# Optimization experiments

Hardware: AMD Instinct MI355X
Metric: run time of the kernel (lower is better)

The kernel has to match this reference:

```python
import jax, jax.numpy as jnp
import numpy as np

LAMBDA_MAX = 2.0  # standard re-scaled Laplacian assumption (DGL lambda_max=[2])
NUM_GRAPHS = 100


def _cheb(feat, src, dst, d_invsqrt, W, b):
    # DGL ChebConv: h = sum_i fc_i(X_i) + b, X_i = Chebyshev recursion on scaled Laplacian
    n = feat.shape[0]
    k = W.shape[0]
    re = 2.0 / LAMBDA_MAX

    def aggr(f):  # D^{-1/2} A D^{-1/2} f  via gather + segment_sum
        fh = f * d_invsqrt
        m = jax.ops.segment_sum(fh[src], dst, num_segments=n)
        return m * d_invsqrt

    X0 = feat
    h = X0 @ W[0]
    if k > 1:
        X1 = -re * aggr(X0) + X0 * (re - 1.0)
        h = h + X1 @ W[1]
        for i in range(2, k):
            Xi = -2.0 * re * aggr(X1) + X1 * (2.0 * (re - 1.0)) - X0
            h = h + Xi @ W[i]
            X0, X1 = X1, Xi
    return h + b


def _edgeconv(feat, src, dst, Wt, bt, Wp, bp):
    # DGL EdgeConv: out_i = max_{j->i} [theta(x_i - x_j) + phi(x_i)], 0 if no in-edges
    n = feat.shape[0]
    theta = (feat[dst] - feat[src]) @ Wt + bt           # [E, H]
    phi = feat @ Wp + bp                                # [N, H]
    msg = theta + phi[dst]                              # [E, H]
    agg = jax.ops.segment_max(msg, dst, num_segments=n)
    return jnp.where(jnp.isfinite(agg), agg, jnp.zeros((), feat.dtype))


def setup_inputs() -> dict:
    key = jax.random.key(0)
    ks = jax.random.split(key, 20)
    N, E, G = 100000, 1600000, NUM_GRAPHS
    IN, H, K = 16, 64, 3

    def lin(k, fan_in, shape):
        return jax.random.normal(k, shape, dtype=jnp.float32) * (1.0 / np.sqrt(fan_in))

    inp = {}
    inp["feat"] = jax.random.normal(ks[0], (N, IN), dtype=jnp.float32)
    inp["src"] = jax.random.randint(ks[1], (E,), 0, N)
    inp["dst"] = jax.random.randint(ks[2], (E,), 0, N)
    inp["graph_ids"] = jnp.sort(jax.random.randint(ks[3], (N,), 0, G))
    # ChebConv params: W [k, in, out], b [out]
    inp["W1"] = lin(ks[4], IN, (K, IN, H)); inp["b1"] = jnp.zeros((H,), jnp.float32)
    inp["W2"] = lin(ks[5], H, (K, H, H));   inp["b2"] = jnp.zeros((H,), jnp.float32)
    inp["W3"] = lin(ks[6], H, (K, H, H));   inp["b3"] = jnp.zeros((H,), jnp.float32)
    # EdgeConv params: theta + phi linears
    inp["Wt1"] = lin(ks[7], H, (H, H));  inp["bt1"] = jnp.zeros((H,), jnp.float32)
    inp["Wp1"] = lin(ks[8], H, (H, H));  inp["bp1"] = jnp.zeros((H,), jnp.float32)
    inp["Wt2"] = lin(ks[9], H, (H, H));  inp["bt2"] = jnp.zeros((H,), jnp.float32)
    inp["Wp2"] = lin(ks[10], H, (H, H)); inp["bp2"] = jnp.zeros((H,), jnp.float32)
    return inp


def reference(feat, src, dst, graph_ids, W1, b1, W2, b2, W3, b3,
              Wt1, bt1, Wp1, bp1, Wt2, bt2, Wp2, bp2):
    n = feat.shape[0]
    deg = jax.ops.segment_sum(jnp.ones((src.shape[0],), feat.dtype), dst, num_segments=n)
    d_invsqrt = (jnp.clip(deg, 1.0, None) ** -0.5)[:, None]  # [N, 1]

    h = jax.nn.relu(_cheb(feat, src, dst, d_invsqrt, W1, b1))
    h = jax.nn.relu(_edgeconv(h, src, dst, Wt1, bt1, Wp1, bp1))
    h = jax.nn.relu(_cheb(h, src, dst, d_invsqrt, W2, b2))
    h = jax.nn.relu(_edgeconv(h, src, dst, Wt2, bt2, Wp2, bp2))
    h = jax.nn.relu(_cheb(h, src, dst, d_invsqrt, W3, b3))

    # dgl.mean_nodes: per-graph mean pooling
    counts = jax.ops.segment_sum(jnp.ones((n,), h.dtype), graph_ids, num_segments=NUM_GRAPHS)
    hg = jax.ops.segment_sum(h, graph_ids, num_segments=NUM_GRAPHS)
    return hg / jnp.clip(counts, 1.0, None)[:, None]
```

## Files before the change

kernel.cpp:

```cpp
#include <hip/hip_runtime.h>
#include <hip/hip_bf16.h>
#include <math.h>

typedef __attribute__((ext_vector_type(8))) short short8;
typedef __attribute__((ext_vector_type(4))) float floatx4;

__device__ __forceinline__ unsigned short bfb(float x) {
    union { __hip_bfloat16 h; unsigned short u; } c;
    c.h = __float2bfloat16(x);
    return c.u;
}
__device__ __forceinline__ float bf2f(unsigned short u) {
    union { unsigned int i; float f; } c;
    c.i = ((unsigned int)u) << 16;
    return c.f;
}
__device__ __forceinline__ unsigned pkmaxu16(unsigned a, unsigned b) {
    unsigned d;
    asm("v_pk_max_u16 %0, %1, %2" : "=v"(d) : "v"(a), "v"(b));
    return d;
}


__global__ __launch_bounds__(256) void k_bhist(const int* __restrict__ dst, int* __restrict__ bcnt, int E) {
    __shared__ int h[512];
    int t = threadIdx.x;
    for (int i = t; i < 512; i += 256) h[i] = 0;
    __syncthreads();
    int step = gridDim.x * 256;
    for (int i = blockIdx.x * 256 + t; i < E; i += step) atomicAdd(&h[dst[i] >> 8], 1);
    __syncthreads();
    for (int i = t; i < 512; i += 256) if (h[i]) atomicAdd(&bcnt[i], h[i]);
}

__global__ __launch_bounds__(512) void k_scanBkt(const int* __restrict__ bcnt, int* __restrict__ boff,
                                                 int* __restrict__ bcur, int nb, int E) {
    __shared__ int s[512];
    int t = threadIdx.x;
    int v = (t < nb) ? bcnt[t] : 0;
    s[t] = v;
    __syncthreads();
    for (int off = 1; off < 512; off <<= 1) {
        int x = (t >= off) ? s[t - off] : 0;
        __syncthreads();
        s[t] += x;
        __syncthreads();
    }
    if (t < nb) { boff[t] = s[t] - v; bcur[t] = s[t] - v; }
    if (t == 0) boff[nb] = E;
}

#define PCHUNK 8192

__global__ __launch_bounds__(256) void k_partA(const int* __restrict__ src, const int* __restrict__ dst,
                                               int* __restrict__ bcur, unsigned* __restrict__ ebuf, int E) {
    __shared__ int h[512];
    __shared__ int base[512];
    int t = threadIdx.x;
    for (int i = t; i < 512; i += 256) h[i] = 0;
    __syncthreads();
    int start = blockIdx.x * PCHUNK;
    int end = start + PCHUNK < E ? start + PCHUNK : E;
    for (int i = start + t; i < end; i += 256) atomicAdd(&h[dst[i] >> 8], 1);
    __syncthreads();
    for (int i = t; i < 512; i += 256) {
        int c = h[i];
        base[i] = c ? atomicAdd(&bcur[i], c) : 0;
        h[i] = 0;
    }
    __syncthreads();
    for (int i = start + t; i < end; i += 256) {
        int d = dst[i];
        int b = d >> 8;
        int r = atomicAdd(&h[b], 1);
        ebuf[base[b] + r] = ((unsigned)src[i] << 8) | (unsigned)(d & 255);
    }
}

__global__ __launch_bounds__(256) void k_finish(const unsigned* __restrict__ ebuf, const int* __restrict__ boff,
                                                int* __restrict__ row_off, float* __restrict__ dinv,
                                                int* __restrict__ csr, int N, int E) {
    __shared__ int h[256];
    __shared__ int sc[256];
    __shared__ int cur[256];
    int b = blockIdx.x, t = threadIdx.x;
    h[t] = 0;
    __syncthreads();
    int beg = boff[b], end = boff[b + 1];
    for (int e = beg + t; e < end; e += 256) atomicAdd(&h[ebuf[e] & 255], 1);
    __syncthreads();
    int v = h[t];
    sc[t] = v;
    __syncthreads();
    for (int off = 1; off < 256; off <<= 1) {
        int x = (t >= off) ? sc[t - off] : 0;
        __syncthreads();
        sc[t] += x;
        __syncthreads();
    }
    int node = (b << 8) + t;
    int excl = beg + sc[t] - v;
    if (node < N) {
        row_off[node] = excl;
        dinv[node] = rsqrtf((float)(v > 1 ? v : 1));
    }
    cur[t] = excl;
    if (b == 0 && t == 0) row_off[N] = E;
    __syncthreads();
    for (int e = beg + t; e < end; e += 256) {
        unsigned ed = ebuf[e];
        int pos = atomicAdd(&cur[ed & 255], 1);
        csr[pos] = (int)(ed >> 8);
    }
}


__global__ __launch_bounds__(256) void k_feat16(const float* __restrict__ feat, const float* __restrict__ dinv,
                                                unsigned short* __restrict__ featd, int total) {
    int i = blockIdx.x * 256 + threadIdx.x;
    if (i < total) featd[i] = bfb(feat[i] * dinv[i >> 4]);
}


__global__ __launch_bounds__(256) void k_aggr16(const unsigned short* __restrict__ Xd, const float* __restrict__ Z,
                                                const float* __restrict__ dinv,
                                                const int* __restrict__ row_off, const int* __restrict__ csr,
                                                float* __restrict__ out, unsigned short* __restrict__ outd,
                                                float alpha, float beta, int N) {
    int node = blockIdx.x * 4 + (threadIdx.x >> 6);
    if (node >= N) return;
    int lane = threadIdx.x & 63;
    int g = lane >> 2;
    int co = (lane & 3) * 8;
    int beg = row_off[node], end = row_off[node + 1];
    int deg = end - beg;
    int myOff = ((lane < deg) ? csr[beg + lane] : 0) << 5;
    int dmain = deg < 64 ? deg : 64;
    float a0 = 0.f, a1 = 0.f, a2 = 0.f, a3 = 0.f;
    int j = 0;
    for (; j + 15 < dmain; j += 16) {
        int off = __shfl(myOff, j + g);
        ushort4 x = *(const ushort4*)((const char*)Xd + off + co);
        a0 += bf2f(x.x); a1 += bf2f(x.y); a2 += bf2f(x.z); a3 += bf2f(x.w);
    }
    if (j < dmain) {
        int idx = j + g;
        int off = __shfl(myOff, idx < dmain ? idx : dmain - 1);
        ushort4 x = *(const ushort4*)((const char*)Xd + off + co);
        if (idx < dmain) {
            a0 += bf2f(x.x); a1 += bf2f(x.y); a2 += bf2f(x.z); a3 += bf2f(x.w);
        }
    }
    for (int e = beg + 64; e < end; e += 16) {
        int idx = e + g;
        int s = csr[idx < end ? idx : end - 1];
        ushort4 x = *(const ushort4*)((const char*)Xd + (s << 5) + co);
        if (idx < end) {
            a0 += bf2f(x.x); a1 += bf2f(x.y); a2 += bf2f(x.z); a3 += bf2f(x.w);
        }
    }
    a0 += __shfl_xor(a0, 4); a0 += __shfl_xor(a0, 8); a0 += __shfl_xor(a0, 16); a0 += __shfl_xor(a0, 32);
    a1 += __shfl_xor(a1, 4); a1 += __shfl_xor(a1, 8); a1 += __shfl_xor(a1, 16); a1 += __shfl_xor(a1, 32);
    a2 += __shfl_xor(a2, 4); a2 += __shfl_xor(a2, 8); a2 += __shfl_xor(a2, 16); a2 += __shfl_xor(a2, 32);
    a3 += __shfl_xor(a3, 4); a3 += __shfl_xor(a3, 8); a3 += __shfl_xor(a3, 16); a3 += __shfl_xor(a3, 32);
    if (g == 0) {
        int c4 = (lane & 3) * 4;
        float dn = dinv[node];
        float v0 = alpha * dn * a0;
        float v1 = alpha * dn * a1;
        float v2 = alpha * dn * a2;
        float v3 = alpha * dn * a3;
        if (Z) {
            float4 zv = *(const float4*)&Z[(size_t)node * 16 + c4];
            v0 += beta * zv.x; v1 += beta * zv.y; v2 += beta * zv.z; v3 += beta * zv.w;
        }
        float4 r = { v0, v1, v2, v3 };
        *(float4*)&out[(size_t)node * 16 + c4] = r;
        if (outd) {
            ushort4 u = { bfb(v0 * dn), bfb(v1 * dn), bfb(v2 * dn), bfb(v3 * dn) };
            *(ushort4*)&outd[(size_t)node * 16 + c4] = u;
        }
    }
}


__global__ __launch_bounds__(256) void k_aggr64(const unsigned short* __restrict__ Xd, const float* __restrict__ Z,
                                                const float* __restrict__ dinv,
                                                const int* __restrict__ row_off, const int* __restrict__ csr,
                                                unsigned short* __restrict__ outb, unsigned short* __restrict__ outd,
                                                float alpha, float beta, int N) {
    int node = blockIdx.x * 4 + (threadIdx.x >> 6);
    if (node >= N) return;
    int lane = threadIdx.x & 63;
    int g = lane >> 4;
    int co = (lane & 15) * 8;
    int beg = row_off[node], end = row_off[node + 1];
    int deg = end - beg;
    int myOff = ((lane < deg) ? csr[beg + lane] : 0) << 7;
    int dmain = deg < 64 ? deg : 64;
    float a0 = 0.f, a1 = 0.f, a2 = 0.f, a3 = 0.f;
    float b0 = 0.f, b1 = 0.f, b2 = 0.f, b3 = 0.f;
    int j = 0;
    for (; j + 15 < dmain; j += 16) {
        int oA = __shfl(myOff, j + g);
        int oB = __shfl(myOff, j + 4 + g);
        int oC = __shfl(myOff, j + 8 + g);
        int oD = __shfl(myOff, j + 12 + g);
        ushort4 xA = *(const ushort4*)((const char*)Xd + oA + co);
        ushort4 xB = *(const ushort4*)((const char*)Xd + oB + co);
        ushort4 xC = *(const ushort4*)((const char*)Xd + oC + co);
        ushort4 xD = *(const ushort4*)((const char*)Xd + oD + co);
        a0 += bf2f(xA.x); a1 += bf2f(xA.y); a2 += bf2f(xA.z); a3 += bf2f(xA.w);
        b0 += bf2f(xB.x); b1 += bf2f(xB.y); b2 += bf2f(xB.z); b3 += bf2f(xB.w);
        a0 += bf2f(xC.x); a1 += bf2f(xC.y); a2 += bf2f(xC.z); a3 += bf2f(xC.w);
        b0 += bf2f(xD.x); b1 += bf2f(xD.y); b2 += bf2f(xD.z); b3 += bf2f(xD.w);
    }
    for (; j + 7 < dmain; j += 8) {
        int oA = __shfl(myOff, j + g);
        int oB = __shfl(myOff, j + 4 + g);
        ushort4 xA = *(const ushort4*)((const char*)Xd + oA + co);
        ushort4 xB = *(const ushort4*)((const char*)Xd + oB + co);
        a0 += bf2f(xA.x); a1 += bf2f(xA.y); a2 += bf2f(xA.z); a3 += bf2f(xA.w);
        b0 += bf2f(xB.x); b1 += bf2f(xB.y); b2 += bf2f(xB.z); b3 += bf2f(xB.w);
    }
    for (; j < dmain; j += 4) {
        int idx = j + g;
        int off = __shfl(myOff, idx < dmain ? idx : dmain - 1);
        ushort4 x = *(const ushort4*)((const char*)Xd + off + co);
        if (idx < dmain) {
            a0 += bf2f(x.x); a1 += bf2f(x.y); a2 += bf2f(x.z); a3 += bf2f(x.w);
        }
    }
    for (int e = beg + 64; e < end; e += 4) {
        int idx = e + g;
        int s = csr[idx < end ? idx : end - 1];
        ushort4 x = *(const ushort4*)((const char*)Xd + (s << 7) + co);
        if (idx < end) {
            a0 += bf2f(x.x); a1 += bf2f(x.y); a2 += bf2f(x.z); a3 += bf2f(x.w);
        }
    }
    a0 += b0; a1 += b1; a2 += b2; a3 += b3;
    a0 += __shfl_xor(a0, 16); a0 += __shfl_xor(a0, 32);
    a1 += __shfl_xor(a1, 16); a1 += __shfl_xor(a1, 32);
    a2 += __shfl_xor(a2, 16); a2 += __shfl_xor(a2, 32);
    a3 += __shfl_xor(a3, 16); a3 += __shfl_xor(a3, 32);
    if (g == 0) {
        int c4 = (lane & 15) * 4;
        float dn = dinv[node];
        float v0 = alpha * dn * a0;
        float v1 = alpha * dn * a1;
        float v2 = alpha * dn * a2;
        float v3 = alpha * dn * a3;
        if (Z) {
            float4 zv = *(const float4*)&Z[(size_t)node * 64 + c4];
            v0 += beta * zv.x; v1 += beta * zv.y; v2 += beta * zv.z; v3 += beta * zv.w;
        }
        ushort4 ub = { bfb(v0), bfb(v1), bfb(v2), bfb(v3) };
        *(ushort4*)&outb[(size_t)node * 64 + c4] = ub;
        if (outd) {
            ushort4 u = { bfb(v0 * dn), bfb(v1 * dn), bfb(v2 * dn), bfb(v3 * dn) };
            *(ushort4*)&outd[(size_t)node * 64 + c4] = u;
        }
    }
}


template <int KDIM, bool BIN16, bool BOUT16>
__global__ __launch_bounds__(256) void k_cheb_m(const float* __restrict__ X0, const void* __restrict__ X1v,
                                                const void* __restrict__ X2v, const float* __restrict__ W,
                                                const float* __restrict__ b, void* __restrict__ outv, int N) {
    constexpr int KT = (KDIM == 16) ? 64 : 3 * KDIM;
    constexpr int SX = KT + 8;
    __shared__ unsigned short Xs[64 * SX];
    __shared__ unsigned short Ws[64 * SX];
    int t = threadIdx.x;

    {
        int sn = t & 63;
        int gn = blockIdx.x * 64 + sn; if (gn >= N) gn = N - 1;
        int k0 = (t >> 6) * (KDIM / 4);
#pragma unroll
        for (int i = 0; i < KDIM / 16; ++i) {
            float4 v = *(const float4*)&X0[(size_t)gn * KDIM + k0 + 4 * i];
            ushort4 u = { bfb(v.x), bfb(v.y), bfb(v.z), bfb(v.w) };
            *(ushort4*)&Xs[sn * SX + k0 + 4 * i] = u;
        }
        if constexpr (BIN16) {
            const unsigned short* X1 = (const unsigned short*)X1v;
            const unsigned short* X2 = (const unsigned short*)X2v;
#pragma unroll
            for (int i = 0; i < KDIM / 16; ++i) {
                *(ushort4*)&Xs[sn * SX + KDIM + k0 + 4 * i] =
                    *(const ushort4*)&X1[(size_t)gn * KDIM + k0 + 4 * i];
                *(ushort4*)&Xs[sn * SX + 2 * KDIM + k0 + 4 * i] =
                    *(const ushort4*)&X2[(size_t)gn * KDIM + k0 + 4 * i];
            }
        } else {
            const float* Xp[2] = { (const float*)X1v, (const float*)X2v };
#pragma unroll
            for (int a = 0; a < 2; ++a) {
#pragma unroll
                for (int i = 0; i < KDIM / 16; ++i) {
                    float4 v = *(const float4*)&Xp[a][(size_t)gn * KDIM + k0 + 4 * i];
                    ushort4 u = { bfb(v.x), bfb(v.y), bfb(v.z), bfb(v.w) };
                    *(ushort4*)&Xs[sn * SX + (a + 1) * KDIM + k0 + 4 * i] = u;
                }
            }
        }
        if (KDIM == 16) {
            int kp = 48 + (t >> 6) * 4;
            ushort4 z = { 0, 0, 0, 0 };
            *(ushort4*)&Xs[sn * SX + kp] = z;
        }
    }
    for (int idx = t; idx < 3 * KDIM * 64; idx += 256) {
        int a = idx / (KDIM * 64);
        int r = idx % (KDIM * 64);
        int k = r >> 6, n = r & 63;
        Ws[n * SX + a * KDIM + k] = bfb(W[idx]);
    }
    if (KDIM == 16) {
        for (int idx = t; idx < 1024; idx += 256) {
            int n = idx & 63, k = 48 + (idx >> 6);
            Ws[n * SX + k] = 0;
        }
    }
    __syncthreads();

    int wave = t >> 6, lane = t & 63;
    int fi = lane & 15, quad = lane >> 4;
    int arow = wave * 16 + fi;

    floatx4 acc0 = {0.f,0.f,0.f,0.f}, acc1 = {0.f,0.f,0.f,0.f}, acc2 = {0.f,0.f,0.f,0.f}, acc3 = {0.f,0.f,0.f,0.f};
#pragma unroll
    for (int ks = 0; ks < KT / 32; ++ks) {
        short8 af = *(const short8*)&Xs[arow * SX + ks * 32 + quad * 8];
        short8 b0 = *(const short8*)&Ws[(0 * 16 + fi) * SX + ks * 32 + quad * 8];
        short8 b1 = *(const short8*)&Ws[(1 * 16 + fi) * SX + ks * 32 + quad * 8];
        short8 b2 = *(const short8*)&Ws[(2 * 16 + fi) * SX + ks * 32 + quad * 8];
        short8 b3 = *(const short8*)&Ws[(3 * 16 + fi) * SX + ks * 32 + quad * 8];
        acc0 = __builtin_amdgcn_mfma_f32_16x16x32_bf16(af, b0, acc0, 0, 0, 0);
        acc1 = __builtin_amdgcn_mfma_f32_16x16x32_bf16(af, b1, acc1, 0, 0, 0);
        acc2 = __builtin_amdgcn_mfma_f32_16x16x32_bf16(af, b2, acc2, 0, 0, 0);
        acc3 = __builtin_amdgcn_mfma_f32_16x16x32_bf16(af, b3, acc3, 0, 0, 0);
    }

    int nbase = blockIdx.x * 64 + wave * 16 + quad * 4;
    floatx4 accs[4] = { acc0, acc1, acc2, acc3 };
#pragma unroll
    for (int nt = 0; nt < 4; ++nt) {
        int col = nt * 16 + fi;
        float bias = b[col];
#pragma unroll
        for (int reg = 0; reg < 4; ++reg) {
            int node = nbase + reg;
            if (node < N) {
                float r = fmaxf(accs[nt][reg] + bias, 0.f);
                if constexpr (BOUT16) {
                    ((unsigned short*)outv)[(size_t)node * 64 + col] = bfb(r);
                } else {
                    ((float*)outv)[(size_t)node * 64 + col] = r;
                }
            }
        }
    }
}


__global__ __launch_bounds__(256) void k_e1_m(const unsigned short* X, const float* __restrict__ Wt,
                                              const float* __restrict__ Wp, const float* __restrict__ bt,
                                              const float* __restrict__ bp,
                                              unsigned short* md, float* __restrict__ pbuf, int N) {
    constexpr int SX = 72;
    __shared__ unsigned short Xs[64 * SX];
    __shared__ unsigned short Ws[128 * SX];
    int t = threadIdx.x;

    {
        int sn = t & 63;
        int gn = blockIdx.x * 64 + sn; if (gn >= N) gn = N - 1;
        int k0 = (t >> 6) * 16;
#pragma unroll
        for (int i = 0; i < 2; ++i) {
            *(short8*)&Xs[sn * SX + k0 + 8 * i] = *(const short8*)&X[(size_t)gn * 64 + k0 + 8 * i];
        }
    }
    for (int idx = t; idx < 4096; idx += 256) {
        int k = idx >> 6, n = idx & 63;
        float wt = Wt[idx];
        Ws[n * SX + k] = bfb(wt);
        Ws[(64 + n) * SX + k] = bfb(wt + Wp[idx]);
    }
    __syncthreads();

    int wave = t >> 6, lane = t & 63;
    int fi = lane & 15, quad = lane >> 4;
    int arow = wave * 16 + fi;

    floatx4 acc[8];
#pragma unroll
    for (int i = 0; i < 8; ++i) acc[i] = (floatx4){0.f,0.f,0.f,0.f};
#pragma unroll
    for (int ks = 0; ks < 2; ++ks) {
        short8 af = *(const short8*)&Xs[arow * SX + ks * 32 + quad * 8];
#pragma unroll
        for (int nt = 0; nt < 8; ++nt) {
            short8 bf = *(const short8*)&Ws[(nt * 16 + fi) * SX + ks * 32 + quad * 8];
            acc[nt] = __builtin_amdgcn_mfma_f32_16x16x32_bf16(af, bf, acc[nt], 0, 0, 0);
        }
    }

    int nbase = blockIdx.x * 64 + wave * 16 + quad * 4;
#pragma unroll
    for (int nt = 0; nt < 8; ++nt) {
        int col = nt * 16 + fi;
        if (col < 64) {
#pragma unroll
            for (int reg = 0; reg < 4; ++reg) {
                int node = nbase + reg;
                if (node < N) {
                    unsigned u = (unsigned)bfb(acc[nt][reg]) ^ 0x8000u;
                    unsigned key = (u & 0x8000u) ? (~u & 0xffffu) : (u | 0x8000u);
                    md[(size_t)node * 64 + col] = (unsigned short)key;
                }
            }
        } else {
            int cc = col - 64;
            float bias = bt[cc] + bp[cc];
#pragma unroll
            for (int reg = 0; reg < 4; ++reg) {
                int node = nbase + reg;
                if (node < N) pbuf[(size_t)node * 64 + cc] = acc[nt][reg] + bias;
            }
        }
    }
}


__global__ __launch_bounds__(256) void k_e2_b(const unsigned short* __restrict__ md, const float* __restrict__ pbuf,
                                              const int* __restrict__ row_off, const int* __restrict__ csr,
                                              const float* __restrict__ dinv, float* __restrict__ out,
                                              unsigned short* __restrict__ outd, int N) {
    int node = blockIdx.x * 4 + (threadIdx.x >> 6);
    if (node >= N) return;
    int lane = threadIdx.x & 63;
    int g = lane >> 4;
    int co = (lane & 15) * 8;
    int beg = row_off[node], end = row_off[node + 1];
    int deg = end - beg;
    int myOff = ((lane < deg) ? csr[beg + lane] : 0) << 7;
    int dmain = deg < 64 ? deg : 64;
    unsigned kA0 = 0, kA1 = 0, kB0 = 0, kB1 = 0;
    int j = 0;
    for (; j + 15 < dmain; j += 16) {
        int oA = __shfl(myOff, j + g);
        int oB = __shfl(myOff, j + 4 + g);
        int oC = __shfl(myOff, j + 8 + g);
        int oD = __shfl(myOff, j + 12 + g);
        uint2 xA = *(const uint2*)((const char*)md + oA + co);
        uint2 xB = *(const uint2*)((const char*)md + oB + co);
        uint2 xC = *(const uint2*)((const char*)md + oC + co);
        uint2 xD = *(const uint2*)((const char*)md + oD + co);
        kA0 = pkmaxu16(kA0, xA.x); kA1 = pkmaxu16(kA1, xA.y);
        kB0 = pkmaxu16(kB0, xB.x); kB1 = pkmaxu16(kB1, xB.y);
        kA0 = pkmaxu16(kA0, xC.x); kA1 = pkmaxu16(kA1, xC.y);
        kB0 = pkmaxu16(kB0, xD.x); kB1 = pkmaxu16(kB1, xD.y);
    }
    for (; j + 7 < dmain; j += 8) {
        int oA = __shfl(myOff, j + g);
        int oB = __shfl(myOff, j + 4 + g);
        uint2 xA = *(const uint2*)((const char*)md + oA + co);
        uint2 xB = *(const uint2*)((const char*)md + oB + co);
        kA0 = pkmaxu16(kA0, xA.x); kA1 = pkmaxu16(kA1, xA.y);
        kB0 = pkmaxu16(kB0, xB.x); kB1 = pkmaxu16(kB1, xB.y);
    }
    for (; j < dmain; j += 4) {
        int idx = j + g;
        int off = __shfl(myOff, idx < dmain ? idx : dmain - 1);
        uint2 x = *(const uint2*)((const char*)md + off + co);
        kA0 = pkmaxu16(kA0, idx < dmain ? x.x : 0u);
        kA1 = pkmaxu16(kA1, idx < dmain ? x.y : 0u);
    }
    for (int e = beg + 64; e < end; e += 4) {
        int idx = e + g;
        int s = csr[idx < end ? idx : end - 1];
        uint2 x = *(const uint2*)((const char*)md + (s << 7) + co);
        kA0 = pkmaxu16(kA0, idx < end ? x.x : 0u);
        kA1 = pkmaxu16(kA1, idx < end ? x.y : 0u);
    }
    kA0 = pkmaxu16(kA0, kB0); kA1 = pkmaxu16(kA1, kB1);
    kA0 = pkmaxu16(kA0, __shfl_xor((int)kA0, 16)); kA0 = pkmaxu16(kA0, __shfl_xor((int)kA0, 32));
    kA1 = pkmaxu16(kA1, __shfl_xor((int)kA1, 16)); kA1 = pkmaxu16(kA1, __shfl_xor((int)kA1, 32));
    if (g == 0) {
        int c4 = (lane & 15) * 4;
        unsigned short ks[4] = { (unsigned short)(kA0 & 0xffff), (unsigned short)(kA0 >> 16),
                                 (unsigned short)(kA1 & 0xffff), (unsigned short)(kA1 >> 16) };
        float a[4];
#pragma unroll
        for (int i = 0; i < 4; ++i) {
            unsigned k = ks[i];
            unsigned short tt = (k & 0x8000u) ? (unsigned short)(k & 0x7fffu) : (unsigned short)(~k & 0xffffu);
            a[i] = bf2f(tt);
        }
        float r0 = 0.f, r1 = 0.f, r2 = 0.f, r3 = 0.f;
        if (end > beg) {
            float4 pv = *(const float4*)&pbuf[(size_t)node * 64 + c4];
            r0 = fmaxf(pv.x + a[0], 0.f);
            r1 = fmaxf(pv.y + a[1], 0.f);
            r2 = fmaxf(pv.z + a[2], 0.f);
            r3 = fmaxf(pv.w + a[3], 0.f);
        }
        float4 r = { r0, r1, r2, r3 };
        *(float4*)&out[(size_t)node * 64 + c4] = r;
        float dn = dinv[node];
        ushort4 u = { bfb(r0 * dn), bfb(r1 * dn), bfb(r2 * dn), bfb(r3 * dn) };
        *(ushort4*)&outd[(size_t)node * 64 + c4] = u;
    }
}


__global__ __launch_bounds__(256) void k_pool(const float* __restrict__ h, const int* __restrict__ gid,
                                              float* __restrict__ out, float* __restrict__ gcnt, int N) {
    const int CHUNK = 128;
    int wave = blockIdx.x * 4 + (threadIdx.x >> 6);
    int lane = threadIdx.x & 63;
    int beg = wave * CHUNK;
    if (beg >= N) return;
    int end = beg + CHUNK < N ? beg + CHUNK : N;
    int gcur = gid[beg];
    float acc = 0.f;
    int cnt = 0;
    for (int n = beg; n < end; ++n) {
        int g = gid[n];
        float v = h[n * 64 + lane];
        if (g != gcur) {
            atomicAdd(&out[gcur * 64 + lane], acc);
            if (lane == 0) atomicAdd(&gcnt[gcur], (float)cnt);
            gcur = g; acc = 0.f; cnt = 0;
        }
        acc += v;
        ++cnt;
    }
    atomicAdd(&out[gcur * 64 + lane], acc);
    if (lane == 0) atomicAdd(&gcnt[gcur], (float)cnt);
}

__global__ __launch_bounds__(256) void k_div(float* __restrict__ out, const float* __restrict__ gcnt, int total) {
    int i = blockIdx.x * blockDim.x + threadIdx.x;
    if (i < total) out[i] /= fmaxf(gcnt[i >> 6], 1.f);
}


extern "C" void kernel_launch(void* const* d_in, const int* in_sizes, int n_in,
                              void* d_out, int out_size, void* d_ws, size_t ws_size,
                              hipStream_t stream) {
    const float* feat = (const float*)d_in[0];
    const int* src = (const int*)d_in[1];
    const int* dst = (const int*)d_in[2];
    const int* gid = (const int*)d_in[3];
    const float* W1 = (const float*)d_in[4];  const float* b1 = (const float*)d_in[5];
    const float* W2 = (const float*)d_in[6];  const float* b2 = (const float*)d_in[7];
    const float* W3 = (const float*)d_in[8];  const float* b3 = (const float*)d_in[9];
    const float* Wt1 = (const float*)d_in[10]; const float* bt1 = (const float*)d_in[11];
    const float* Wp1 = (const float*)d_in[12]; const float* bp1 = (const float*)d_in[13];
    const float* Wt2 = (const float*)d_in[14]; const float* bt2 = (const float*)d_in[15];
    const float* Wp2 = (const float*)d_in[16]; const float* bp2 = (const float*)d_in[17];
    float* out = (float*)d_out;

    const int N = in_sizes[0] / 16;
    const int E = in_sizes[1];
    const int G = out_size / 64;
    const int nb = (N + 255) >> 8;

    char* p = (char*)d_ws;
    auto alloc = [&](size_t nbytes) {
        void* r = (void*)p;
        p += (nbytes + 255) & ~(size_t)255;
        return r;
    };
    int* row_off  = (int*)alloc((size_t)(N + 1) * 4);
    int* csr      = (int*)alloc((size_t)E * 4);
    int* bcnt     = (int*)alloc(512 * 4);
    int* boff     = (int*)alloc(513 * 4);
    int* bcur     = (int*)alloc(512 * 4);
    float* dinv   = (float*)alloc((size_t)N * 4);
    float* bufA   = (float*)alloc((size_t)N * 64 * 4);
    float* bufB   = (float*)alloc((size_t)N * 64 * 4);
    float* bufC   = (float*)alloc((size_t)N * 64 * 4);
    float* bufD   = (float*)alloc((size_t)N * 64 * 4);
    unsigned short* md = (unsigned short*)alloc((size_t)N * 64 * 2);
    float* gcnt   = (float*)alloc((size_t)G * 4);

    unsigned* ebuf = (unsigned*)bufA;
    unsigned short* hd = (unsigned short*)bufC;
    unsigned short* xd = (unsigned short*)bufC + (size_t)N * 64;
    unsigned short* hb = md;

    hipMemsetAsync(bcnt, 0, 512 * 4, stream);
    hipMemsetAsync(gcnt, 0, (size_t)G * 4, stream);
    hipMemsetAsync(d_out, 0, (size_t)out_size * 4, stream);

    const int nb16 = (N * 16 + 255) / 256;
    const int nbw = (N + 3) / 4;
    const int npool = ((N + 127) / 128 + 3) / 4;
    const int nbt = (N + 63) / 64;
    const int npart = (E + PCHUNK - 1) / PCHUNK;

    k_bhist<<<256, 256, 0, stream>>>(dst, bcnt, E);
    k_scanBkt<<<1, 512, 0, stream>>>(bcnt, boff, bcur, nb, E);
    k_partA<<<npart, 256, 0, stream>>>(src, dst, bcur, ebuf, E);
    k_finish<<<nb, 256, 0, stream>>>(ebuf, boff, row_off, dinv, csr, N, E);

    k_feat16<<<nb16, 256, 0, stream>>>(feat, dinv, hd, N * 16);
    k_aggr16<<<nbw, 256, 0, stream>>>(hd, nullptr, dinv, row_off, csr, bufA, xd, -1.f, 0.f, N);
    k_aggr16<<<nbw, 256, 0, stream>>>(xd, feat, dinv, row_off, csr, bufB, nullptr, -2.f, -1.f, N);
    k_cheb_m<16, false, true><<<nbt, 256, 0, stream>>>(feat, bufA, bufB, W1, b1, hb, N);

    k_e1_m<<<nbt, 256, 0, stream>>>(hb, Wt1, Wp1, bt1, bp1, md, bufB, N);
    k_e2_b<<<nbw, 256, 0, stream>>>(md, bufB, row_off, csr, dinv, bufD, hd, N);

    k_aggr64<<<nbw, 256, 0, stream>>>(hd, nullptr, dinv, row_off, csr, (unsigned short*)bufA, xd, -1.f, 0.f, N);
    k_aggr64<<<nbw, 256, 0, stream>>>(xd, bufD, dinv, row_off, csr, (unsigned short*)bufB, nullptr, -2.f, -1.f, N);
    k_cheb_m<64, true, true><<<nbt, 256, 0, stream>>>(bufD, bufA, bufB, W2, b2, hb, N);

    k_e1_m<<<nbt, 256, 0, stream>>>(hb, Wt2, Wp2, bt2, bp2, md, bufB, N);
    k_e2_b<<<nbw, 256, 0, stream>>>(md, bufB, row_off, csr, dinv, bufD, hd, N);

    k_aggr64<<<nbw, 256, 0, stream>>>(hd, nullptr, dinv, row_off, csr, (unsigned short*)bufA, xd, -1.f, 0.f, N);
    k_aggr64<<<nbw, 256, 0, stream>>>(xd, bufD, dinv, row_off, csr, (unsigned short*)bufB, nullptr, -2.f, -1.f, N);
    k_cheb_m<64, true, false><<<nbt, 256, 0, stream>>>(bufD, bufA, bufB, W3, b3, bufC, N);

    k_pool<<<npool, 256, 0, stream>>>(bufC, gid, out, gcnt, N);
    k_div<<<(out_size + 255) / 256, 256, 0, stream>>>(out, gcnt, out_size);
}
```

Measured before the change: 621.3 us.

## Widen gather loads to 16 bytes, use zero-page padding, store edge output as bf16

The 64-wide aggregation and edge-max kernels now let each lane load 16 bytes per neighbor (8 lanes per row) instead of 8 bytes. Lanes past the degree point at a zeroed scratch page, so the first 32 neighbors are gathered unconditionally without masking. The edge-conv output and the Chebyshev X0 input are now stored in bf16 rather than fp32, which halves that traffic. The aim is fewer, wider memory transactions and less branching, at the cost of wasted loads for nodes with few neighbors and some extra bf16 rounding.

```diff
diff --git a/kernel.cpp b/kernel.cpp
--- a/kernel.cpp
+++ b/kernel.cpp
@@ -14,6 +14,12 @@
     union { unsigned int i; float f; } c;
     c.i = ((unsigned int)u) << 16;
     return c.f;
+}
+__device__ __forceinline__ void acc2(float& lo, float& hi, unsigned d) {
+    union { unsigned u; float f; } a, b;
+    a.u = d << 16;
+    b.u = d & 0xffff0000u;
+    lo += a.f; hi += b.f;
 }
 __device__ __forceinline__ unsigned pkmaxu16(unsigned a, unsigned b) {
     unsigned d;
@@ -126,7 +132,7 @@
                                                 const float* __restrict__ dinv,
                                                 const int* __restrict__ row_off, const int* __restrict__ csr,
                                                 float* __restrict__ out, unsigned short* __restrict__ outd,
-                                                float alpha, float beta, int N) {
+                                                float alpha, float beta, int zoff, int N) {
     int node = blockIdx.x * 4 + (threadIdx.x >> 6);
     if (node >= N) return;
     int lane = threadIdx.x & 63;
@@ -134,29 +140,31 @@
     int co = (lane & 3) * 8;
     int beg = row_off[node], end = row_off[node + 1];
     int deg = end - beg;
-    int myOff = ((lane < deg) ? csr[beg + lane] : 0) << 5;
-    int dmain = deg < 64 ? deg : 64;
+    int myOff = (lane < deg) ? (csr[beg + lane] << 5) : zoff;
+    const char* base = (const char*)Xd + co;
     float a0 = 0.f, a1 = 0.f, a2 = 0.f, a3 = 0.f;
-    int j = 0;
-    for (; j + 15 < dmain; j += 16) {
-        int off = __shfl(myOff, j + g);
-        ushort4 x = *(const ushort4*)((const char*)Xd + off + co);
-        a0 += bf2f(x.x); a1 += bf2f(x.y); a2 += bf2f(x.z); a3 += bf2f(x.w);
-    }
-    if (j < dmain) {
-        int idx = j + g;
-        int off = __shfl(myOff, idx < dmain ? idx : dmain - 1);
-        ushort4 x = *(const ushort4*)((const char*)Xd + off + co);
-        if (idx < dmain) {
+    {
+        int o0 = __shfl(myOff, g);
+        int o1 = __shfl(myOff, 16 + g);
+        ushort4 x0 = *(const ushort4*)(base + o0);
+        ushort4 x1 = *(const ushort4*)(base + o1);
+        a0 += bf2f(x0.x); a1 += bf2f(x0.y); a2 += bf2f(x0.z); a3 += bf2f(x0.w);
+        a0 += bf2f(x1.x); a1 += bf2f(x1.y); a2 += bf2f(x1.z); a3 += bf2f(x1.w);
+    }
+    if (deg > 32) {
+        int dmain = deg < 64 ? deg : 64;
+        for (int j = 32; j < dmain; j += 16) {
+            int o = __shfl(myOff, j + g);
+            ushort4 x = *(const ushort4*)(base + o);
             a0 += bf2f(x.x); a1 += bf2f(x.y); a2 += bf2f(x.z); a3 += bf2f(x.w);
         }
-    }
-    for (int e = beg + 64; e < end; e += 16) {
-        int idx = e + g;
-        int s = csr[idx < end ? idx : end - 1];
-        ushort4 x = *(const ushort4*)((const char*)Xd + (s << 5) + co);
-        if (idx < end) {
-            a0 += bf2f(x.x); a1 += bf2f(x.y); a2 += bf2f(x.z); a3 += bf2f(x.w);
+        for (int e = beg + 64; e < end; e += 16) {
+            int idx = e + g;
+            int s = csr[idx < end ? idx : end - 1];
+            ushort4 x = *(const ushort4*)(base + (s << 5));
+            if (idx < end) {
+                a0 += bf2f(x.x); a1 += bf2f(x.y); a2 += bf2f(x.z); a3 += bf2f(x.w);
+            }
         }
     }
     a0 += __shfl_xor(a0, 4); a0 += __shfl_xor(a0, 8); a0 += __shfl_xor(a0, 16); a0 += __shfl_xor(a0, 32);
@@ -184,89 +192,93 @@
 }
 
 
-__global__ __launch_bounds__(256) void k_aggr64(const unsigned short* __restrict__ Xd, const float* __restrict__ Z,
+__global__ __launch_bounds__(256) void k_aggr64(const unsigned short* __restrict__ Xd,
+                                                const unsigned short* __restrict__ Z,
                                                 const float* __restrict__ dinv,
                                                 const int* __restrict__ row_off, const int* __restrict__ csr,
                                                 unsigned short* __restrict__ outb, unsigned short* __restrict__ outd,
-                                                float alpha, float beta, int N) {
+                                                float alpha, float beta, int zoff, int N) {
     int node = blockIdx.x * 4 + (threadIdx.x >> 6);
     if (node >= N) return;
     int lane = threadIdx.x & 63;
-    int g = lane >> 4;
-    int co = (lane & 15) * 8;
+    int g = lane >> 3;
+    int co = (lane & 7) * 16;
     int beg = row_off[node], end = row_off[node + 1];
     int deg = end - beg;
-    int myOff = ((lane < deg) ? csr[beg + lane] : 0) << 7;
-    int dmain = deg < 64 ? deg : 64;
-    float a0 = 0.f, a1 = 0.f, a2 = 0.f, a3 = 0.f;
-    float b0 = 0.f, b1 = 0.f, b2 = 0.f, b3 = 0.f;
-    int j = 0;
-    for (; j + 15 < dmain; j += 16) {
-        int oA = __shfl(myOff, j + g);
-        int oB = __shfl(myOff, j + 4 + g);
-        int oC = __shfl(myOff, j + 8 + g);
-        int oD = __shfl(myOff, j + 12 + g);
-        ushort4 xA = *(const ushort4*)((const char*)Xd + oA + co);
-        ushort4 xB = *(const ushort4*)((const char*)Xd + oB + co);
-        ushort4 xC = *(const ushort4*)((const char*)Xd + oC + co);
-        ushort4 xD = *(const ushort4*)((const char*)Xd + oD + co);
-        a0 += bf2f(xA.x); a1 += bf2f(xA.y); a2 += bf2f(xA.z); a3 += bf2f(xA.w);
-        b0 += bf2f(xB.x); b1 += bf2f(xB.y); b2 += bf2f(xB.z); b3 += bf2f(xB.w);
-        a0 += bf2f(xC.x); a1 += bf2f(xC.y); a2 += bf2f(xC.z); a3 += bf2f(xC.w);
-        b0 += bf2f(xD.x); b1 += bf2f(xD.y); b2 += bf2f(xD.z); b3 += bf2f(xD.w);
-    }
-    for (; j + 7 < dmain; j += 8) {
-        int oA = __shfl(myOff, j + g);
-        int oB = __shfl(myOff, j + 4 + g);
-        ushort4 xA = *(const ushort4*)((const char*)Xd + oA + co);
-        ushort4 xB = *(const ushort4*)((const char*)Xd + oB + co);
-        a0 += bf2f(xA.x); a1 += bf2f(xA.y); a2 += bf2f(xA.z); a3 += bf2f(xA.w);
-        b0 += bf2f(xB.x); b1 += bf2f(xB.y); b2 += bf2f(xB.z); b3 += bf2f(xB.w);
-    }
-    for (; j < dmain; j += 4) {
-        int idx = j + g;
-        int off = __shfl(myOff, idx < dmain ? idx : dmain - 1);
-        ushort4 x = *(const ushort4*)((const char*)Xd + off + co);
-        if (idx < dmain) {
-            a0 += bf2f(x.x); a1 += bf2f(x.y); a2 += bf2f(x.z); a3 += bf2f(x.w);
-        }
-    }
-    for (int e = beg + 64; e < end; e += 4) {
-        int idx = e + g;
-        int s = csr[idx < end ? idx : end - 1];
-        ushort4 x = *(const ushort4*)((const char*)Xd + (s << 7) + co);
-        if (idx < end) {
-            a0 += bf2f(x.x); a1 += bf2f(x.y); a2 += bf2f(x.z); a3 += bf2f(x.w);
-        }
-    }
-    a0 += b0; a1 += b1; a2 += b2; a3 += b3;
-    a0 += __shfl_xor(a0, 16); a0 += __shfl_xor(a0, 32);
-    a1 += __shfl_xor(a1, 16); a1 += __shfl_xor(a1, 32);
-    a2 += __shfl_xor(a2, 16); a2 += __shfl_xor(a2, 32);
-    a3 += __shfl_xor(a3, 16); a3 += __shfl_xor(a3, 32);
+    int myOff = (lane < deg) ? (csr[beg + lane] << 7) : zoff;
+    const char* base = (const char*)Xd + co;
+    float a0 = 0.f, a1 = 0.f, a2 = 0.f, a3 = 0.f, a4 = 0.f, a5 = 0.f, a6 = 0.f, a7 = 0.f;
+    {
+        int o0 = __shfl(myOff, g);
+        int o1 = __shfl(myOff, 8 + g);
+        int o2 = __shfl(myOff, 16 + g);
+        int o3 = __shfl(myOff, 24 + g);
+        uint4 x0 = *(const uint4*)(base + o0);
+        uint4 x1 = *(const uint4*)(base + o1);
+        uint4 x2 = *(const uint4*)(base + o2);
+        uint4 x3 = *(const uint4*)(base + o3);
+        acc2(a0, a1, x0.x); acc2(a2, a3, x0.y); acc2(a4, a5, x0.z); acc2(a6, a7, x0.w);
+        acc2(a0, a1, x1.x); acc2(a2, a3, x1.y); acc2(a4, a5, x1.z); acc2(a6, a7, x1.w);
+        acc2(a0, a1, x2.x); acc2(a2, a3, x2.y); acc2(a4, a5, x2.z); acc2(a6, a7, x2.w);
+        acc2(a0, a1, x3.x); acc2(a2, a3, x3.y); acc2(a4, a5, x3.z); acc2(a6, a7, x3.w);
+    }
+    if (deg > 32) {
+        int dmain = deg < 64 ? deg : 64;
+        for (int j = 32; j < dmain; j += 8) {
+            int o = __shfl(myOff, j + g);
+            uint4 x = *(const uint4*)(base + o);
+            acc2(a0, a1, x.x); acc2(a2, a3, x.y); acc2(a4, a5, x.z); acc2(a6, a7, x.w);
+        }
+        for (int e = beg + 64; e < end; e += 8) {
+            int idx = e + g;
+            int s = csr[idx < end ? idx : end - 1];
+            uint4 x = *(const uint4*)(base + (s << 7));
+            if (idx < end) {
+                acc2(a0, a1, x.x); acc2(a2, a3, x.y); acc2(a4, a5, x.z); acc2(a6, a7, x.w);
+            }
+        }
+    }
+    a0 += __shfl_xor(a0, 8); a0 += __shfl_xor(a0, 16); a0 += __shfl_xor(a0, 32);
+    a1 += __shfl_xor(a1, 8); a1 += __shfl_xor(a1, 16); a1 += __shfl_xor(a1, 32);
+    a2 += __shfl_xor(a2, 8); a2 += __shfl_xor(a2, 16); a2 += __shfl_xor(a2, 32);
+    a3 += __shfl_xor(a3, 8); a3 += __shfl_xor(a3, 16); a3 += __shfl_xor(a3, 32);
+    a4 += __shfl_xor(a4, 8); a4 += __shfl_xor(a4, 16); a4 += __shfl_xor(a4, 32);
+    a5 += __shfl_xor(a5, 8); a5 += __shfl_xor(a5, 16); a5 += __shfl_xor(a5, 32);
+    a6 += __shfl_xor(a6, 8); a6 += __shfl_xor(a6, 16); a6 += __shfl_xor(a6, 32);
+    a7 += __shfl_xor(a7, 8); a7 += __shfl_xor(a7, 16); a7 += __shfl_xor(a7, 32);
     if (g == 0) {
-        int c4 = (lane & 15) * 4;
         float dn = dinv[node];
-        float v0 = alpha * dn * a0;
-        float v1 = alpha * dn * a1;
-        float v2 = alpha * dn * a2;
-        float v3 = alpha * dn * a3;
+        float v[8] = { a0, a1, a2, a3, a4, a5, a6, a7 };
+#pragma unroll
+        for (int i = 0; i < 8; ++i) v[i] *= alpha * dn;
+        size_t rb = (size_t)node * 128 + co;
         if (Z) {
-            float4 zv = *(const float4*)&Z[(size_t)node * 64 + c4];
-            v0 += beta * zv.x; v1 += beta * zv.y; v2 += beta * zv.z; v3 += beta * zv.w;
-        }
-        ushort4 ub = { bfb(v0), bfb(v1), bfb(v2), bfb(v3) };
-        *(ushort4*)&outb[(size_t)node * 64 + c4] = ub;
-        if (outd) {
-            ushort4 u = { bfb(v0 * dn), bfb(v1 * dn), bfb(v2 * dn), bfb(v3 * dn) };
-            *(ushort4*)&outd[(size_t)node * 64 + c4] = u;
-        }
+            uint4 zv = *(const uint4*)((const char*)Z + rb);
+            unsigned zd[4] = { zv.x, zv.y, zv.z, zv.w };
+#pragma unroll
+            for (int i = 0; i < 4; ++i) {
+                union { unsigned u; float f; } lo, hi;
+                lo.u = zd[i] << 16; hi.u = zd[i] & 0xffff0000u;
+                v[2 * i] += beta * lo.f;
+                v[2 * i + 1] += beta * hi.f;
+            }
+        }
+        uint4 ub, ud;
+        unsigned* pb = (unsigned*)&ub;
+        unsigned* pd = (unsigned*)&ud;
+#pragma unroll
+        for (int i = 0; i < 4; ++i) {
+            pb[i] = (unsigned)bfb(v[2 * i]) | ((unsigned)bfb(v[2 * i + 1]) << 16);
+            pd[i] = (unsigned)bfb(v[2 * i] * dn) | ((unsigned)bfb(v[2 * i + 1] * dn) << 16);
+        }
+        *(uint4*)((char*)outb + rb) = ub;
+        if (outd) *(uint4*)((char*)outd + rb) = ud;
     }
 }
 
 
 template <int KDIM, bool BIN16, bool BOUT16>
-__global__ __launch_bounds__(256) void k_cheb_m(const float* __restrict__ X0, const void* __restrict__ X1v,
+__global__ __launch_bounds__(256) void k_cheb_m(const void* __restrict__ X0v, const void* __restrict__ X1v,
                                                 const void* __restrict__ X2v, const float* __restrict__ W,
                                                 const float* __restrict__ b, void* __restrict__ outv, int N) {
     constexpr int KT = (KDIM == 16) ? 64 : 3 * KDIM;
@@ -279,31 +291,26 @@
         int sn = t & 63;
         int gn = blockIdx.x * 64 + sn; if (gn >= N) gn = N - 1;
         int k0 = (t >> 6) * (KDIM / 4);
-#pragma unroll
-        for (int i = 0; i < KDIM / 16; ++i) {
-            float4 v = *(const float4*)&X0[(size_t)gn * KDIM + k0 + 4 * i];
-            ushort4 u = { bfb(v.x), bfb(v.y), bfb(v.z), bfb(v.w) };
-            *(ushort4*)&Xs[sn * SX + k0 + 4 * i] = u;
-        }
         if constexpr (BIN16) {
-            const unsigned short* X1 = (const unsigned short*)X1v;
-            const unsigned short* X2 = (const unsigned short*)X2v;
-#pragma unroll
-            for (int i = 0; i < KDIM / 16; ++i) {
-                *(ushort4*)&Xs[sn * SX + KDIM + k0 + 4 * i] =
-                    *(const ushort4*)&X1[(size_t)gn * KDIM + k0 + 4 * i];
-                *(ushort4*)&Xs[sn * SX + 2 * KDIM + k0 + 4 * i] =
-                    *(const ushort4*)&X2[(size_t)gn * KDIM + k0 + 4 * i];
+            const unsigned short* Xp[3] = { (const unsigned short*)X0v, (const unsigned short*)X1v,
+                                            (const unsigned short*)X2v };
+#pragma unroll
+            for (int a = 0; a < 3; ++a) {
+#pragma unroll
+                for (int i = 0; i < KDIM / 16; ++i) {
+                    *(ushort4*)&Xs[sn * SX + a * KDIM + k0 + 4 * i] =
+                        *(const ushort4*)&Xp[a][(size_t)gn * KDIM + k0 + 4 * i];
+                }
             }
         } else {
-            const float* Xp[2] = { (const float*)X1v, (const float*)X2v };
-#pragma unroll
-            for (int a = 0; a < 2; ++a) {
+            const float* Xp[3] = { (const float*)X0v, (const float*)X1v, (const float*)X2v };
+#pragma unroll
+            for (int a = 0; a < 3; ++a) {
 #pragma unroll
                 for (int i = 0; i < KDIM / 16; ++i) {
                     float4 v = *(const float4*)&Xp[a][(size_t)gn * KDIM + k0 + 4 * i];
                     ushort4 u = { bfb(v.x), bfb(v.y), bfb(v.z), bfb(v.w) };
-                    *(ushort4*)&Xs[sn * SX + (a + 1) * KDIM + k0 + 4 * i] = u;
+                    *(ushort4*)&Xs[sn * SX + a * KDIM + k0 + 4 * i] = u;
                 }
             }
         }
@@ -331,7 +338,7 @@
     int fi = lane & 15, quad = lane >> 4;
     int arow = wave * 16 + fi;
 
-    floatx4 acc0 = {0.f,0.f,0.f,0.f}, acc1 = {0.f,0.f,0.f,0.f}, acc2 = {0.f,0.f,0.f,0.f}, acc3 = {0.f,0.f,0.f,0.f};
+    floatx4 acc0 = {0.f,0.f,0.f,0.f}, acc1 = {0.f,0.f,0.f,0.f}, acc2v = {0.f,0.f,0.f,0.f}, acc3 = {0.f,0.f,0.f,0.f};
 #pragma unroll
     for (int ks = 0; ks < KT / 32; ++ks) {
         short8 af = *(const short8*)&Xs[arow * SX + ks * 32 + quad * 8];
@@ -341,12 +348,12 @@
         short8 b3 = *(const short8*)&Ws[(3 * 16 + fi) * SX + ks * 32 + quad * 8];
         acc0 = __builtin_amdgcn_mfma_f32_16x16x32_bf16(af, b0, acc0, 0, 0, 0);
         acc1 = __builtin_amdgcn_mfma_f32_16x16x32_bf16(af, b1, acc1, 0, 0, 0);
-        acc2 = __builtin_amdgcn_mfma_f32_16x16x32_bf16(af, b2, acc2, 0, 0, 0);
+        acc2v = __builtin_amdgcn_mfma_f32_16x16x32_bf16(af, b2, acc2v, 0, 0, 0);
         acc3 = __builtin_amdgcn_mfma_f32_16x16x32_bf16(af, b3, acc3, 0, 0, 0);
     }
 
     int nbase = blockIdx.x * 64 + wave * 16 + quad * 4;
-    floatx4 accs[4] = { acc0, acc1, acc2, acc3 };
+    floatx4 accs[4] = { acc0, acc1, acc2v, acc3 };
 #pragma unroll
     for (int nt = 0; nt < 4; ++nt) {
         int col = nt * 16 + fi;
@@ -439,82 +446,87 @@
 
 __global__ __launch_bounds__(256) void k_e2_b(const unsigned short* __restrict__ md, const float* __restrict__ pbuf,
                                               const int* __restrict__ row_off, const int* __restrict__ csr,
-                                              const float* __restrict__ dinv, float* __restrict__ out,
-                                              unsigned short* __restrict__ outd, int N) {
+                                              const float* __restrict__ dinv, unsigned short* __restrict__ out,
+                                              unsigned short* __restrict__ outd, int zoff, int N) {
     int node = blockIdx.x * 4 + (threadIdx.x >> 6);
     if (node >= N) return;
     int lane = threadIdx.x & 63;
-    int g = lane >> 4;
-    int co = (lane & 15) * 8;
+    int g = lane >> 3;
+    int co = (lane & 7) * 16;
     int beg = row_off[node], end = row_off[node + 1];
     int deg = end - beg;
-    int myOff = ((lane < deg) ? csr[beg + lane] : 0) << 7;
     int dmain = deg < 64 ? deg : 64;
-    unsigned kA0 = 0, kA1 = 0, kB0 = 0, kB1 = 0;
-    int j = 0;
-    for (; j + 15 < dmain; j += 16) {
-        int oA = __shfl(myOff, j + g);
-        int oB = __shfl(myOff, j + 4 + g);
-        int oC = __shfl(myOff, j + 8 + g);
-        int oD = __shfl(myOff, j + 12 + g);
-        uint2 xA = *(const uint2*)((const char*)md + oA + co);
-        uint2 xB = *(const uint2*)((const char*)md + oB + co);
-        uint2 xC = *(const uint2*)((const char*)md + oC + co);
-        uint2 xD = *(const uint2*)((const char*)md + oD + co);
-        kA0 = pkmaxu16(kA0, xA.x); kA1 = pkmaxu16(kA1, xA.y);
-        kB0 = pkmaxu16(kB0, xB.x); kB1 = pkmaxu16(kB1, xB.y);
-        kA0 = pkmaxu16(kA0, xC.x); kA1 = pkmaxu16(kA1, xC.y);
-        kB0 = pkmaxu16(kB0, xD.x); kB1 = pkmaxu16(kB1, xD.y);
-    }
-    for (; j + 7 < dmain; j += 8) {
-        int oA = __shfl(myOff, j + g);
-        int oB = __shfl(myOff, j + 4 + g);
-        uint2 xA = *(const uint2*)((const char*)md + oA + co);
-        uint2 xB = *(const uint2*)((const char*)md + oB + co);
-        kA0 = pkmaxu16(kA0, xA.x); kA1 = pkmaxu16(kA1, xA.y);
-        kB0 = pkmaxu16(kB0, xB.x); kB1 = pkmaxu16(kB1, xB.y);
-    }
-    for (; j < dmain; j += 4) {
-        int idx = j + g;
-        int off = __shfl(myOff, idx < dmain ? idx : dmain - 1);
-        uint2 x = *(const uint2*)((const char*)md + off + co);
-        kA0 = pkmaxu16(kA0, idx < dmain ? x.x : 0u);
-        kA1 = pkmaxu16(kA1, idx < dmain ? x.y : 0u);
-    }
-    for (int e = beg + 64; e < end; e += 4) {
-        int idx = e + g;
-        int s = csr[idx < end ? idx : end - 1];
-        uint2 x = *(const uint2*)((const char*)md + (s << 7) + co);
-        kA0 = pkmaxu16(kA0, idx < end ? x.x : 0u);
-        kA1 = pkmaxu16(kA1, idx < end ? x.y : 0u);
-    }
-    kA0 = pkmaxu16(kA0, kB0); kA1 = pkmaxu16(kA1, kB1);
-    kA0 = pkmaxu16(kA0, __shfl_xor((int)kA0, 16)); kA0 = pkmaxu16(kA0, __shfl_xor((int)kA0, 32));
-    kA1 = pkmaxu16(kA1, __shfl_xor((int)kA1, 16)); kA1 = pkmaxu16(kA1, __shfl_xor((int)kA1, 32));
+    int li = lane < dmain ? lane : dmain - 1;
+    int myOff = (deg > 0) ? (csr[beg + li] << 7) : zoff;
+    const char* base = (const char*)md + co;
+    unsigned k0 = 0, k1 = 0, k2 = 0, k3 = 0;
+    {
+        int o0 = __shfl(myOff, g);
+        int o1 = __shfl(myOff, 8 + g);
+        int o2 = __shfl(myOff, 16 + g);
+        int o3 = __shfl(myOff, 24 + g);
+        uint4 x0 = *(const uint4*)(base + o0);
+        uint4 x1 = *(const uint4*)(base + o1);
+        uint4 x2 = *(const uint4*)(base + o2);
+        uint4 x3 = *(const uint4*)(base + o3);
+        k0 = pkmaxu16(k0, x0.x); k1 = pkmaxu16(k1, x0.y); k2 = pkmaxu16(k2, x0.z); k3 = pkmaxu16(k3, x0.w);
+        k0 = pkmaxu16(k0, x1.x); k1 = pkmaxu16(k1, x1.y); k2 = pkmaxu16(k2, x1.z); k3 = pkmaxu16(k3, x1.w);
+        k0 = pkmaxu16(k0, x2.x); k1 = pkmaxu16(k1, x2.y); k2 = pkmaxu16(k2, x2.z); k3 = pkmaxu16(k3, x2.w);
+        k0 = pkmaxu16(k0, x3.x); k1 = pkmaxu16(k1, x3.y); k2 = pkmaxu16(k2, x3.z); k3 = pkmaxu16(k3, x3.w);
+    }
+    if (deg > 32) {
+        for (int j = 32; j < dmain; j += 8) {
+            int o = __shfl(myOff, j + g);
+            uint4 x = *(const uint4*)(base + o);
+            k0 = pkmaxu16(k0, x.x); k1 = pkmaxu16(k1, x.y); k2 = pkmaxu16(k2, x.z); k3 = pkmaxu16(k3, x.w);
+        }
+        for (int e = beg + 64; e < end; e += 8) {
+            int idx = e + g;
+            int s = csr[idx < end ? idx : end - 1];
+            uint4 x = *(const uint4*)(base + (s << 7));
+            k0 = pkmaxu16(k0, x.x); k1 = pkmaxu16(k1, x.y); k2 = pkmaxu16(k2, x.z); k3 = pkmaxu16(k3, x.w);
+        }
+    }
+    k0 = pkmaxu16(k0, __shfl_xor((int)k0, 8)); k0 = pkmaxu16(k0, __shfl_xor((int)k0, 16)); k0 = pkmaxu16(k0, __shfl_xor((int)k0, 32));
+    k1 = pkmaxu16(k1, __shfl_xor((int)k1, 8)); k1 = pkmaxu16(k1, __shfl_xor((int)k1, 16)); k1 = pkmaxu16(k1, __shfl_xor((int)k1, 32));
+    k2 = pkmaxu16(k2, __shfl_xor((int)k2, 8)); k2 = pkmaxu16(k2, __shfl_xor((int)k2, 16)); k2 = pkmaxu16(k2, __shfl_xor((int)k2, 32));
+    k3 = pkmaxu16(k3, __shfl_xor((int)k3, 8)); k3 = pkmaxu16(k3, __shfl_xor((int)k3, 16)); k3 = pkmaxu16(k3, __shfl_xor((int)k3, 32));
     if (g == 0) {
-        int c4 = (lane & 15) * 4;
-        unsigned short ks[4] = { (unsigned short)(kA0 & 0xffff), (unsigned short)(kA0 >> 16),
-                                 (unsigned short)(kA1 & 0xffff), (unsigned short)(kA1 >> 16) };
-        float a[4];
+        unsigned kd[4] = { k0, k1, k2, k3 };
+        float a[8];
 #pragma unroll
         for (int i = 0; i < 4; ++i) {
-            unsigned k = ks[i];
-            unsigned short tt = (k & 0x8000u) ? (unsigned short)(k & 0x7fffu) : (unsigned short)(~k & 0xffffu);
-            a[i] = bf2f(tt);
-        }
-        float r0 = 0.f, r1 = 0.f, r2 = 0.f, r3 = 0.f;
+            unsigned klo = kd[i] & 0xffffu, khi = kd[i] >> 16;
+            unsigned short tlo = (klo & 0x8000u) ? (unsigned short)(klo & 0x7fffu) : (unsigned short)(~klo & 0xffffu);
+            unsigned short thi = (khi & 0x8000u) ? (unsigned short)(khi & 0x7fffu) : (unsigned short)(~khi & 0xffffu);
+            a[2 * i] = bf2f(tlo);
+            a[2 * i + 1] = bf2f(thi);
+        }
+        float r[8];
         if (end > beg) {
-            float4 pv = *(const float4*)&pbuf[(size_t)node * 64 + c4];
-            r0 = fmaxf(pv.x + a[0], 0.f);
-            r1 = fmaxf(pv.y + a[1], 0.f);
-            r2 = fmaxf(pv.z + a[2], 0.f);
-            r3 = fmaxf(pv.w + a[3], 0.f);
-        }
-        float4 r = { r0, r1, r2, r3 };
-        *(float4*)&out[(size_t)node * 64 + c4] = r;
+            const float* pv = &pbuf[(size_t)node * 64 + (lane & 7) * 8];
+            float4 p0 = *(const float4*)pv;
+            float4 p1 = *(const float4*)(pv + 4);
+            r[0] = fmaxf(p0.x + a[0], 0.f); r[1] = fmaxf(p0.y + a[1], 0.f);
+            r[2] = fmaxf(p0.z + a[2], 0.f); r[3] = fmaxf(p0.w + a[3], 0.f);
+            r[4] = fmaxf(p1.x + a[4], 0.f); r[5] = fmaxf(p1.y + a[5], 0.f);
+            r[6] = fmaxf(p1.z + a[6], 0.f); r[7] = fmaxf(p1.w + a[7], 0.f);
+        } else {
+#pragma unroll
+            for (int i = 0; i < 8; ++i) r[i] = 0.f;
+        }
         float dn = dinv[node];
-        ushort4 u = { bfb(r0 * dn), bfb(r1 * dn), bfb(r2 * dn), bfb(r3 * dn) };
-        *(ushort4*)&outd[(size_t)node * 64 + c4] = u;
+        size_t rb = (size_t)node * 128 + co;
+        uint4 ub, ud;
+        unsigned* pb = (unsigned*)&ub;
+        unsigned* pd = (unsigned*)&ud;
+#pragma unroll
+        for (int i = 0; i < 4; ++i) {
+            pb[i] = (unsigned)bfb(r[2 * i]) | ((unsigned)bfb(r[2 * i + 1]) << 16);
+            pd[i] = (unsigned)bfb(r[2 * i] * dn) | ((unsigned)bfb(r[2 * i + 1] * dn) << 16);
+        }
+        *(uint4*)((char*)out + rb) = ub;
+        *(uint4*)((char*)outd + rb) = ud;
     }
 }
 
@@ -584,6 +596,7 @@
     int* boff     = (int*)alloc(513 * 4);
     int* bcur     = (int*)alloc(512 * 4);
     float* dinv   = (float*)alloc((size_t)N * 4);
+    char* zpage   = (char*)alloc(256);
     float* bufA   = (float*)alloc((size_t)N * 64 * 4);
     float* bufB   = (float*)alloc((size_t)N * 64 * 4);
     float* bufC   = (float*)alloc((size_t)N * 64 * 4);
@@ -595,8 +608,14 @@
     unsigned short* hd = (unsigned short*)bufC;
     unsigned short* xd = (unsigned short*)bufC + (size_t)N * 64;
     unsigned short* hb = md;
+    unsigned short* hD = (unsigned short*)bufD;
+
+    const int zo_hd = (int)((char*)zpage - (char*)hd);
+    const int zo_xd = (int)((char*)zpage - (char*)xd);
+    const int zo_md = (int)((char*)zpage - (char*)md);
 
     hipMemsetAsync(bcnt, 0, 512 * 4, stream);
+    hipMemsetAsync(zpage, 0, 256, stream);
     hipMemsetAsync(gcnt, 0, (size_t)G * 4, stream);
     hipMemsetAsync(d_out, 0, (size_t)out_size * 4, stream);
 
@@ -612,23 +631,23 @@
     k_finish<<<nb, 256, 0, stream>>>(ebuf, boff, row_off, dinv, csr, N, E);
 
     k_feat16<<<nb16, 256, 0, stream>>>(feat, dinv, hd, N * 16);
-    k_aggr16<<<nbw, 256, 0, stream>>>(hd, nullptr, dinv, row_off, csr, bufA, xd, -1.f, 0.f, N);
-    k_aggr16<<<nbw, 256, 0, stream>>>(xd, feat, dinv, row_off, csr, bufB, nullptr, -2.f, -1.f, N);
+    k_aggr16<<<nbw, 256, 0, stream>>>(hd, nullptr, dinv, row_off, csr, bufA, xd, -1.f, 0.f, zo_hd, N);
+    k_aggr16<<<nbw, 256, 0, stream>>>(xd, feat, dinv, row_off, csr, bufB, nullptr, -2.f, -1.f, zo_xd, N);
     k_cheb_m<16, false, true><<<nbt, 256, 0, stream>>>(feat, bufA, bufB, W1, b1, hb, N);
 
     k_e1_m<<<nbt, 256, 0, stream>>>(hb, Wt1, Wp1, bt1, bp1, md, bufB, N);
-    k_e2_b<<<nbw, 256, 0, stream>>>(md, bufB, row_off, csr, dinv, bufD, hd, N);
-
-    k_aggr64<<<nbw, 256, 0, stream>>>(hd, nullptr, dinv, row_off, csr, (unsigned short*)bufA, xd, -1.f, 0.f, N);
-    k_aggr64<<<nbw, 256, 0, stream>>>(xd, bufD, dinv, row_off, csr, (unsigned short*)bufB, nullptr, -2.f, -1.f, N);
-    k_cheb_m<64, true, true><<<nbt, 256, 0, stream>>>(bufD, bufA, bufB, W2, b2, hb, N);
+    k_e2_b<<<nbw, 256, 0, stream>>>(md, bufB, row_off, csr, dinv, hD, hd, zo_md, N);
+
+    k_aggr64<<<nbw, 256, 0, stream>>>(hd, nullptr, dinv, row_off, csr, (unsigned short*)bufA, xd, -1.f, 0.f, zo_hd, N);
+    k_aggr64<<<nbw, 256, 0, stream>>>(xd, hD, dinv, row_off, csr, (unsigned short*)bufB, nullptr, -2.f, -1.f, zo_xd, N);
+    k_cheb_m<64, true, true><<<nbt, 256, 0, stream>>>(hD, bufA, bufB, W2, b2, hb, N);
 
     k_e1_m<<<nbt, 256, 0, stream>>>(hb, Wt2, Wp2, bt2, bp2, md, bufB, N);
-    k_e2_b<<<nbw, 256, 0, stream>>>(md, bufB, row_off, csr, dinv, bufD, hd, N);
-
-    k_aggr64<<<nbw, 256, 0, stream>>>(hd, nullptr, dinv, row_off, csr, (unsigned short*)bufA, xd, -1.f, 0.f, N);
-    k_aggr64<<<nbw, 256, 0, stream>>>(xd, bufD, dinv, row_off, csr, (unsigned short*)bufB, nullptr, -2.f, -1.f, N);
-    k_cheb_m<64, true, false><<<nbt, 256, 0, stream>>>(bufD, bufA, bufB, W3, b3, bufC, N);
+    k_e2_b<<<nbw, 256, 0, stream>>>(md, bufB, row_off, csr, dinv, hD, hd, zo_md, N);
+
+    k_aggr64<<<nbw, 256, 0, stream>>>(hd, nullptr, dinv, row_off, csr, (unsigned short*)bufA, xd, -1.f, 0.f, zo_hd, N);
+    k_aggr64<<<nbw, 256, 0, stream>>>(xd, hD, dinv, row_off, csr, (unsigned short*)bufB, nullptr, -2.f, -1.f, zo_xd, N);
+    k_cheb_m<64, true, false><<<nbt, 256, 0, stream>>>(hD, bufA, bufB, W3, b3, bufC, N);
 
     k_pool<<<npool, 256, 0, stream>>>(bufC, gid, out, gcnt, N);
     k_div<<<(out_size + 255) / 256, 256, 0, stream>>>(out, gcnt, out_size);
```

Measured after the change: 595.2 us. -4.2%, faster.
